# Kernel tuning notes

Hardware: AMD Instinct MI355X
Metric: run time of the kernel (lower is better)

The kernel has to match this reference:

```python
import jax, jax.numpy as jnp
import numpy as np
from jax import lax

T, B, H = 8192, 16, 256
D0, D1, D2 = 64, 64, 128


def setup_inputs() -> dict:
    key = jax.random.key(0)
    ks = jax.random.split(key, 16)
    k = 1.0 / np.sqrt(H)  # torch LSTMCell default init scale

    def u(kk, shape):
        return jax.random.uniform(kk, shape, jnp.float32, -k, k)

    inp = {
        "x0": jax.random.normal(ks[0], (T, B, D0), jnp.float32),
        "x1": jax.random.normal(ks[1], (T // 2, B, D1), jnp.float32),
        "x2": jax.random.normal(ks[2], (T // 4, B, D2), jnp.float32),
    }
    # one LSTMCell per possible concatenated input size: a=256 (all), b=128 (two), c=64 (one)
    sizes = [("a", D0 + D1 + D2), ("b", D0 + D1), ("c", D0)]
    i = 3
    for name, s in sizes:
        inp[f"W_ih_{name}"] = u(ks[i], (4 * H, s)); i += 1
        inp[f"W_hh_{name}"] = u(ks[i], (4 * H, H)); i += 1
        inp[f"b_ih_{name}"] = u(ks[i], (4 * H,)); i += 1
        inp[f"b_hh_{name}"] = u(ks[i], (4 * H,)); i += 1
    return inp


def _cell(x, h, c, Wih, Whh, bih, bhh):
    # torch.nn.LSTMCell: gates = x W_ih^T + b_ih + h W_hh^T + b_hh; order i,f,g,o
    g = x @ Wih.T + bih + h @ Whh.T + bhh
    i, f, gg, o = jnp.split(g, 4, axis=-1)
    c2 = jax.nn.sigmoid(f) * c + jax.nn.sigmoid(i) * jnp.tanh(gg)
    h2 = jax.nn.sigmoid(o) * jnp.tanh(c2)
    return h2, c2


def reference(x0, x1, x2,
              W_ih_a, W_hh_a, b_ih_a, b_hh_a,
              W_ih_b, W_hh_b, b_ih_b, b_hh_b,
              W_ih_c, W_hh_c, b_ih_c, b_hh_c):
    # ratios = [1, 2, 4]; active sets are nested: t%4==0 -> all 3, t%2==0 -> first 2, else first only
    def step(carry, t):
        h, c = carry

        def br_all(_):
            xt = jnp.concatenate([x0[t], x1[t // 2], x2[t // 4]], axis=-1)  # [B, 256]
            return _cell(xt, h, c, W_ih_a, W_hh_a, b_ih_a, b_hh_a)

        def br_two(_):
            xt = jnp.concatenate([x0[t], x1[t // 2]], axis=-1)  # [B, 128]
            return _cell(xt, h, c, W_ih_b, W_hh_b, b_ih_b, b_hh_b)

        def br_one(_):
            return _cell(x0[t], h, c, W_ih_c, W_hh_c, b_ih_c, b_hh_c)  # [B, 64]

        branch = jnp.where(t % 4 == 0, 0, jnp.where(t % 2 == 0, 1, 2))
        h2, c2 = lax.switch(branch, [br_all, br_two, br_one], None)
        return (h2, c2), h2

    h0 = jnp.zeros((B, H), jnp.float32)
    (_, _), ys = lax.scan(step, (h0, h0), jnp.arange(T))
    return ys  # [T, B, H]
```

## Files before the change

kernel.cpp:

```cpp
#include <hip/hip_runtime.h>
#include <stdint.h>


typedef _Float16 half8 __attribute__((ext_vector_type(8)));
typedef float floatx4 __attribute__((ext_vector_type(4)));

#define T_STEPS 8192
#define NWG 16

__device__ __forceinline__ float fsig(float x) {
    return __builtin_amdgcn_rcpf(1.0f + __expf(-x));
}
__device__ __forceinline__ float ftanh(float x) {
    return 1.0f - 2.0f * __builtin_amdgcn_rcpf(1.0f + __expf(2.0f * x));
}

__device__ __forceinline__ half8 ld8w(const float* p) {
    floatx4 a = *(const floatx4*)p;
    floatx4 b = *(const floatx4*)(p + 4);
    half8 h;
    h[0] = (_Float16)a[0]; h[1] = (_Float16)a[1]; h[2] = (_Float16)a[2]; h[3] = (_Float16)a[3];
    h[4] = (_Float16)b[0]; h[5] = (_Float16)b[1]; h[6] = (_Float16)b[2]; h[7] = (_Float16)b[3];
    return h;
}

__global__ void init_ws_kernel(uint32_t* ws) {
    for (int i = threadIdx.x; i < 5120; i += 256) ws[i] = 0;
}

__global__ __launch_bounds__(256, 1) void lstm_kernel(
    const float* __restrict__ x0, const float* __restrict__ x1, const float* __restrict__ x2,
    const float* __restrict__ Wih_a, const float* __restrict__ Whh_a,
    const float* __restrict__ bih_a, const float* __restrict__ bhh_a,
    const float* __restrict__ Wih_b, const float* __restrict__ Whh_b,
    const float* __restrict__ bih_b, const float* __restrict__ bhh_b,
    const float* __restrict__ Wih_c, const float* __restrict__ Whh_c,
    const float* __restrict__ bih_c, const float* __restrict__ bhh_c,
    float* __restrict__ out, uint8_t* __restrict__ ws)
{
    const int tid = threadIdx.x;
    const int g   = blockIdx.x;
    const int w   = tid >> 6;
    const int l   = tid & 63;
    const int n   = l & 15;
    const int mg  = l >> 4;
    const int up  = n & 3;
    const int gt  = n >> 2;
    const int unit = g * 16 + w * 4 + up;
    const int R    = gt * 256 + unit;

    int* flags = (int*)ws;
    _Float16* buf0 = (_Float16*)(ws + 4096);
    _Float16* buf1 = (_Float16*)(ws + 4096 + 8192);

    __shared__ _Float16 XH[16][520];

    half8 wfa[16], wfb[12], wfc[10];
    {
        const int ko = mg * 8;
        #pragma unroll
        for (int kt = 0; kt < 8; ++kt) wfa[kt]     = ld8w(Wih_a + (size_t)R * 256 + kt * 32 + ko);
        #pragma unroll
        for (int kt = 0; kt < 8; ++kt) wfa[8 + kt] = ld8w(Whh_a + (size_t)R * 256 + kt * 32 + ko);
        #pragma unroll
        for (int kt = 0; kt < 4; ++kt) wfb[kt]     = ld8w(Wih_b + (size_t)R * 128 + kt * 32 + ko);
        #pragma unroll
        for (int kt = 0; kt < 8; ++kt) wfb[4 + kt] = ld8w(Whh_b + (size_t)R * 256 + kt * 32 + ko);
        #pragma unroll
        for (int kt = 0; kt < 2; ++kt) wfc[kt]     = ld8w(Wih_c + (size_t)R * 64  + kt * 32 + ko);
        #pragma unroll
        for (int kt = 0; kt < 8; ++kt) wfc[2 + kt] = ld8w(Whh_c + (size_t)R * 256 + kt * 32 + ko);
    }
    const float ba = bih_a[R] + bhh_a[R];
    const float bb = bih_b[R] + bhh_b[R];
    const float bc = bih_c[R] + bhh_c[R];

    float cst[4] = {0.f, 0.f, 0.f, 0.f};

    for (int t = 0; t < T_STEPS; ++t) {
        __syncthreads();
        if (tid == 0)
            __hip_atomic_store(&flags[g * 32], t, __ATOMIC_RELEASE, __HIP_MEMORY_SCOPE_AGENT);

        const int br = ((t & 3) == 0) ? 0 : (((t & 1) == 0) ? 1 : 2);
        const int kx = (br == 0) ? 256 : ((br == 1) ? 128 : 64);

        if (tid < 128) {
            const int m = tid >> 3, cg = (tid & 7) * 8;
            *(half8*)&XH[m][cg] = ld8w(x0 + (size_t)t * 1024 + m * 64 + cg);
        } else if (br < 2) {
            const int tt = tid - 128;
            const int m = tt >> 3, cg = (tt & 7) * 8;
            *(half8*)&XH[m][64 + cg] = ld8w(x1 + (size_t)(t >> 1) * 1024 + m * 64 + cg);
        }
        if (br == 0) {
            const int m = tid >> 4, cg = (tid & 15) * 8;
            *(half8*)&XH[m][128 + cg] = ld8w(x2 + (size_t)(t >> 2) * 2048 + m * 128 + cg);
        }

        if (w == 0) {
            if (l < NWG) {
                while (__hip_atomic_load(&flags[l * 32], __ATOMIC_RELAXED,
                                         __HIP_MEMORY_SCOPE_AGENT) < t) { }
            }
            __builtin_amdgcn_fence(__ATOMIC_ACQUIRE, "agent");
        }
        __syncthreads();

        {
            const _Float16* hb = ((t & 1) == 0) ? buf1 : buf0;
            const int m = tid >> 4, cg = (tid & 15) * 16;
            uint4 q0 = *(const uint4*)(hb + m * 256 + cg);
            uint4 q1 = *(const uint4*)(hb + m * 256 + cg + 8);
            *(uint4*)&XH[m][kx + cg]     = q0;
            *(uint4*)&XH[m][kx + cg + 8] = q1;
        }
        __syncthreads();

        floatx4 acc = {0.f, 0.f, 0.f, 0.f};
        {
            const int ao = mg * 8;
            if (br == 0) {
                #pragma unroll
                for (int kt = 0; kt < 16; ++kt)
                    acc = __builtin_amdgcn_mfma_f32_16x16x32_f16(
                        *(const half8*)&XH[n][kt * 32 + ao], wfa[kt], acc, 0, 0, 0);
            } else if (br == 1) {
                #pragma unroll
                for (int kt = 0; kt < 12; ++kt)
                    acc = __builtin_amdgcn_mfma_f32_16x16x32_f16(
                        *(const half8*)&XH[n][kt * 32 + ao], wfb[kt], acc, 0, 0, 0);
            } else {
                #pragma unroll
                for (int kt = 0; kt < 10; ++kt)
                    acc = __builtin_amdgcn_mfma_f32_16x16x32_f16(
                        *(const half8*)&XH[n][kt * 32 + ao], wfc[kt], acc, 0, 0, 0);
            }
        }

        const float bsel = (br == 0) ? ba : ((br == 1) ? bb : bc);
        float h2v[4];
        const int b0 = l & ~12;
        #pragma unroll
        for (int r = 0; r < 4; ++r) {
            const float gv = acc[r] + bsel;
            const float vi = __shfl(gv, b0,      64);
            const float vf = __shfl(gv, b0 + 4,  64);
            const float vg = __shfl(gv, b0 + 8,  64);
            const float vo = __shfl(gv, b0 + 12, 64);
            const float c2 = fsig(vf) * cst[r] + fsig(vi) * ftanh(vg);
            cst[r] = c2;
            h2v[r] = fsig(vo) * ftanh(c2);
        }

        if ((l & 12) == 0) {
            float* op = out + (size_t)t * 4096 + (size_t)(mg * 4) * 256 + unit;
            #pragma unroll
            for (int r = 0; r < 4; ++r) op[r * 256] = h2v[r];
        }

        {
            _Float16* hw = (t & 1) ? buf1 : buf0;
            const int s0 = l & ~15;
            #pragma unroll
            for (int r = 0; r < 4; ++r) {
                const unsigned hv =
                    (unsigned)__builtin_bit_cast(unsigned short, (_Float16)h2v[r]);
                const unsigned v0 = (unsigned)__shfl((int)hv, s0,     64);
                const unsigned v1 = (unsigned)__shfl((int)hv, s0 + 1, 64);
                const unsigned v2 = (unsigned)__shfl((int)hv, s0 + 2, 64);
                const unsigned v3 = (unsigned)__shfl((int)hv, s0 + 3, 64);
                if (n == 0) {
                    const unsigned long long pk =
                          (unsigned long long)(v0 & 0xffffu)
                        | ((unsigned long long)(v1 & 0xffffu) << 16)
                        | ((unsigned long long)(v2 & 0xffffu) << 32)
                        | ((unsigned long long)(v3 & 0xffffu) << 48);
                    *(unsigned long long*)(hw + (size_t)(mg * 4 + r) * 256 + g * 16 + w * 4) = pk;
                }
            }
        }
    }
}

extern "C" void kernel_launch(void* const* d_in, const int* in_sizes, int n_in,
                              void* d_out, int out_size, void* d_ws, size_t ws_size,
                              hipStream_t stream) {
    (void)in_sizes; (void)n_in; (void)out_size; (void)ws_size;
    hipLaunchKernelGGL(init_ws_kernel, dim3(1), dim3(256), 0, stream, (uint32_t*)d_ws);
    hipLaunchKernelGGL(lstm_kernel, dim3(NWG), dim3(256), 0, stream,
        (const float*)d_in[0], (const float*)d_in[1], (const float*)d_in[2],
        (const float*)d_in[3], (const float*)d_in[4], (const float*)d_in[5], (const float*)d_in[6],
        (const float*)d_in[7], (const float*)d_in[8], (const float*)d_in[9], (const float*)d_in[10],
        (const float*)d_in[11], (const float*)d_in[12], (const float*)d_in[13], (const float*)d_in[14],
        (float*)d_out, (uint8_t*)d_ws);
}
```

Measured before the change: 23.47 ms.

## Replace flag barrier with timestamp-tagged hidden-state ring buffer polling

Drops the per-step flag store and spin-wait. Each block now writes its new hidden-state slice with the step index packed beside the data, using sc1 global stores into a ring of up to 4 slots. Consumers poll the data itself until every tag matches, which removes a separate barrier round-trip and the init kernel. Also splits the MFMA chain into two accumulators, applies sigmoid/tanh before the gate shuffles, and moves the output store after the state publish. The risks are that stale tags in an uninitialized workspace could falsely match, and that the extra polling traffic has its own cost.

```diff
diff --git a/kernel.cpp b/kernel.cpp
--- a/kernel.cpp
+++ b/kernel.cpp
@@ -4,6 +4,7 @@
 
 typedef _Float16 half8 __attribute__((ext_vector_type(8)));
 typedef float floatx4 __attribute__((ext_vector_type(4)));
+typedef unsigned int u32x4 __attribute__((ext_vector_type(4)));
 
 #define T_STEPS 8192
 #define NWG 16
@@ -24,8 +25,19 @@
     return h;
 }
 
-__global__ void init_ws_kernel(uint32_t* ws) {
-    for (int i = threadIdx.x; i < 5120; i += 256) ws[i] = 0;
+__device__ __forceinline__ void ld64_sc1(const void* p, u32x4& a, u32x4& b, u32x4& c, u32x4& d) {
+    asm volatile(
+        "global_load_dwordx4 %0, %4, off sc1\n\t"
+        "global_load_dwordx4 %1, %4, off offset:16 sc1\n\t"
+        "global_load_dwordx4 %2, %4, off offset:32 sc1\n\t"
+        "global_load_dwordx4 %3, %4, off offset:48 sc1\n\t"
+        "s_waitcnt vmcnt(0)"
+        : "=&v"(a), "=&v"(b), "=&v"(c), "=&v"(d)
+        : "v"(p)
+        : "memory");
+}
+__device__ __forceinline__ void st16_sc1(void* p, u32x4 v) {
+    asm volatile("global_store_dwordx4 %0, %1, off sc1" :: "v"(p), "v"(v) : "memory");
 }
 
 __global__ __launch_bounds__(256, 1) void lstm_kernel(
@@ -36,7 +48,7 @@
     const float* __restrict__ bih_b, const float* __restrict__ bhh_b,
     const float* __restrict__ Wih_c, const float* __restrict__ Whh_c,
     const float* __restrict__ bih_c, const float* __restrict__ bhh_c,
-    float* __restrict__ out, uint8_t* __restrict__ ws)
+    float* __restrict__ out, uint8_t* __restrict__ ws, int smask)
 {
     const int tid = threadIdx.x;
     const int g   = blockIdx.x;
@@ -49,9 +61,7 @@
     const int unit = g * 16 + w * 4 + up;
     const int R    = gt * 256 + unit;
 
-    int* flags = (int*)ws;
-    _Float16* buf0 = (_Float16*)(ws + 4096);
-    _Float16* buf1 = (_Float16*)(ws + 4096 + 8192);
+    uint8_t* hring = ws;
 
     __shared__ _Float16 XH[16][520];
 
@@ -79,8 +89,6 @@
 
     for (int t = 0; t < T_STEPS; ++t) {
         __syncthreads();
-        if (tid == 0)
-            __hip_atomic_store(&flags[g * 32], t, __ATOMIC_RELEASE, __HIP_MEMORY_SCOPE_AGENT);
 
         const int br = ((t & 3) == 0) ? 0 : (((t & 1) == 0) ? 1 : 2);
         const int kx = (br == 0) ? 256 : ((br == 1) ? 128 : 64);
@@ -98,69 +106,84 @@
             *(half8*)&XH[m][128 + cg] = ld8w(x2 + (size_t)(t >> 2) * 2048 + m * 128 + cg);
         }
 
-        if (w == 0) {
-            if (l < NWG) {
-                while (__hip_atomic_load(&flags[l * 32], __ATOMIC_RELAXED,
-                                         __HIP_MEMORY_SCOPE_AGENT) < t) { }
+        {
+            const int row = tid >> 4, u = tid & 15;
+            _Float16* dst = &XH[row][kx + u * 16];
+            if (t == 0) {
+                *(u32x4*)dst       = (u32x4)0u;
+                *(u32x4*)(dst + 8) = (u32x4)0u;
+            } else {
+                const uint32_t want = (uint32_t)(t - 1);
+                const uint8_t* src = hring + (size_t)((t - 1) & smask) * 16384
+                                   + (size_t)row * 1024 + (size_t)u * 64;
+                u32x4 a, b, c, d;
+                for (;;) {
+                    ld64_sc1(src, a, b, c, d);
+                    if (a[1] == want && a[3] == want && b[1] == want && b[3] == want &&
+                        c[1] == want && c[3] == want && d[1] == want && d[3] == want)
+                        break;
+                }
+                u32x4 lo = {a[0], a[2], b[0], b[2]};
+                u32x4 hi = {c[0], c[2], d[0], d[2]};
+                *(u32x4*)dst       = lo;
+                *(u32x4*)(dst + 8) = hi;
             }
-            __builtin_amdgcn_fence(__ATOMIC_ACQUIRE, "agent");
         }
         __syncthreads();
 
-        {
-            const _Float16* hb = ((t & 1) == 0) ? buf1 : buf0;
-            const int m = tid >> 4, cg = (tid & 15) * 16;
-            uint4 q0 = *(const uint4*)(hb + m * 256 + cg);
-            uint4 q1 = *(const uint4*)(hb + m * 256 + cg + 8);
-            *(uint4*)&XH[m][kx + cg]     = q0;
-            *(uint4*)&XH[m][kx + cg + 8] = q1;
-        }
-        __syncthreads();
-
-        floatx4 acc = {0.f, 0.f, 0.f, 0.f};
+        floatx4 ac0 = {0.f, 0.f, 0.f, 0.f}, ac1 = {0.f, 0.f, 0.f, 0.f};
         {
             const int ao = mg * 8;
             if (br == 0) {
                 #pragma unroll
-                for (int kt = 0; kt < 16; ++kt)
-                    acc = __builtin_amdgcn_mfma_f32_16x16x32_f16(
-                        *(const half8*)&XH[n][kt * 32 + ao], wfa[kt], acc, 0, 0, 0);
+                for (int kt = 0; kt < 16; kt += 2) {
+                    ac0 = __builtin_amdgcn_mfma_f32_16x16x32_f16(
+                        *(const half8*)&XH[n][kt * 32 + ao], wfa[kt], ac0, 0, 0, 0);
+                    ac1 = __builtin_amdgcn_mfma_f32_16x16x32_f16(
+                        *(const half8*)&XH[n][(kt + 1) * 32 + ao], wfa[kt + 1], ac1, 0, 0, 0);
+                }
             } else if (br == 1) {
                 #pragma unroll
-                for (int kt = 0; kt < 12; ++kt)
-                    acc = __builtin_amdgcn_mfma_f32_16x16x32_f16(
-                        *(const half8*)&XH[n][kt * 32 + ao], wfb[kt], acc, 0, 0, 0);
+                for (int kt = 0; kt < 12; kt += 2) {
+                    ac0 = __builtin_amdgcn_mfma_f32_16x16x32_f16(
+                        *(const half8*)&XH[n][kt * 32 + ao], wfb[kt], ac0, 0, 0, 0);
+                    ac1 = __builtin_amdgcn_mfma_f32_16x16x32_f16(
+                        *(const half8*)&XH[n][(kt + 1) * 32 + ao], wfb[kt + 1], ac1, 0, 0, 0);
+                }
             } else {
                 #pragma unroll
-                for (int kt = 0; kt < 10; ++kt)
-                    acc = __builtin_amdgcn_mfma_f32_16x16x32_f16(
-                        *(const half8*)&XH[n][kt * 32 + ao], wfc[kt], acc, 0, 0, 0);
+                for (int kt = 0; kt < 10; kt += 2) {
+                    ac0 = __builtin_amdgcn_mfma_f32_16x16x32_f16(
+                        *(const half8*)&XH[n][kt * 32 + ao], wfc[kt], ac0, 0, 0, 0);
+                    ac1 = __builtin_amdgcn_mfma_f32_16x16x32_f16(
+                        *(const half8*)&XH[n][(kt + 1) * 32 + ao], wfc[kt + 1], ac1, 0, 0, 0);
+                }
             }
         }
+        const floatx4 acc = ac0 + ac1;
 
         const float bsel = (br == 0) ? ba : ((br == 1) ? bb : bc);
+        float tv[4];
+        #pragma unroll
+        for (int r = 0; r < 4; ++r) {
+            const float gv = acc[r] + bsel;
+            tv[r] = (gt == 2) ? ftanh(gv) : fsig(gv);
+        }
         float h2v[4];
         const int b0 = l & ~12;
         #pragma unroll
         for (int r = 0; r < 4; ++r) {
-            const float gv = acc[r] + bsel;
-            const float vi = __shfl(gv, b0,      64);
-            const float vf = __shfl(gv, b0 + 4,  64);
-            const float vg = __shfl(gv, b0 + 8,  64);
-            const float vo = __shfl(gv, b0 + 12, 64);
-            const float c2 = fsig(vf) * cst[r] + fsig(vi) * ftanh(vg);
+            const float vi = __shfl(tv[r], b0,      64);
+            const float vf = __shfl(tv[r], b0 + 4,  64);
+            const float vg = __shfl(tv[r], b0 + 8,  64);
+            const float vo = __shfl(tv[r], b0 + 12, 64);
+            const float c2 = vf * cst[r] + vi * vg;
             cst[r] = c2;
-            h2v[r] = fsig(vo) * ftanh(c2);
-        }
-
-        if ((l & 12) == 0) {
-            float* op = out + (size_t)t * 4096 + (size_t)(mg * 4) * 256 + unit;
-            #pragma unroll
-            for (int r = 0; r < 4; ++r) op[r * 256] = h2v[r];
+            h2v[r] = vo * ftanh(c2);
         }
 
         {
-            _Float16* hw = (t & 1) ? buf1 : buf0;
+            uint8_t* sb = hring + (size_t)(t & smask) * 16384 + (size_t)(8 * g + 2 * w) * 8;
             const int s0 = l & ~15;
             #pragma unroll
             for (int r = 0; r < 4; ++r) {
@@ -171,14 +194,17 @@
                 const unsigned v2 = (unsigned)__shfl((int)hv, s0 + 2, 64);
                 const unsigned v3 = (unsigned)__shfl((int)hv, s0 + 3, 64);
                 if (n == 0) {
-                    const unsigned long long pk =
-                          (unsigned long long)(v0 & 0xffffu)
-                        | ((unsigned long long)(v1 & 0xffffu) << 16)
-                        | ((unsigned long long)(v2 & 0xffffu) << 32)
-                        | ((unsigned long long)(v3 & 0xffffu) << 48);
-                    *(unsigned long long*)(hw + (size_t)(mg * 4 + r) * 256 + g * 16 + w * 4) = pk;
+                    u32x4 pk = { (v0 & 0xffffu) | (v1 << 16), (unsigned)t,
+                                 (v2 & 0xffffu) | (v3 << 16), (unsigned)t };
+                    st16_sc1(sb + (size_t)(mg * 4 + r) * 1024, pk);
                 }
             }
+        }
+
+        if (gt == 0) {
+            float* op = out + (size_t)t * 4096 + (size_t)(mg * 4) * 256 + unit;
+            #pragma unroll
+            for (int r = 0; r < 4; ++r) op[r * 256] = h2v[r];
         }
     }
 }
@@ -186,12 +212,12 @@
 extern "C" void kernel_launch(void* const* d_in, const int* in_sizes, int n_in,
                               void* d_out, int out_size, void* d_ws, size_t ws_size,
                               hipStream_t stream) {
-    (void)in_sizes; (void)n_in; (void)out_size; (void)ws_size;
-    hipLaunchKernelGGL(init_ws_kernel, dim3(1), dim3(256), 0, stream, (uint32_t*)d_ws);
+    (void)in_sizes; (void)n_in; (void)out_size;
+    const int smask = (ws_size >= 4 * 16384) ? 3 : 1;
     hipLaunchKernelGGL(lstm_kernel, dim3(NWG), dim3(256), 0, stream,
         (const float*)d_in[0], (const float*)d_in[1], (const float*)d_in[2],
         (const float*)d_in[3], (const float*)d_in[4], (const float*)d_in[5], (const float*)d_in[6],
         (const float*)d_in[7], (const float*)d_in[8], (const float*)d_in[9], (const float*)d_in[10],
         (const float*)d_in[11], (const float*)d_in[12], (const float*)d_in[13], (const float*)d_in[14],
-        (float*)d_out, (uint8_t*)d_ws);
-}
+        (float*)d_out, (uint8_t*)d_ws, smask);
+}
```

After: 19.78 ms. 15.7% less time.
